# Performance work log

Measured on AMD Instinct MI355X. Metric: run time of the kernel, lower is better.

The kernel has to match this reference:

```python
import jax, jax.numpy as jnp
import numpy as np

N_NODES = 50000
N_EDGES = 800000
F_IN = 128
HIDDEN = 128
N_CLASSES = 10
N_GRAPHS = 256


def _glorot(key, shape):
    lim = float(np.sqrt(6.0 / (shape[0] + shape[1])))
    return jax.random.uniform(key, shape, jnp.float32, -lim, lim)


def setup_inputs() -> dict:
    key = jax.random.key(0)
    ks = jax.random.split(key, 12)
    x = jax.random.normal(ks[0], (N_NODES, F_IN), jnp.float32)
    edge_index = jax.random.randint(ks[1], (2, N_EDGES), 0, N_NODES, jnp.int64)
    batch = jnp.sort(jax.random.randint(ks[2], (N_NODES,), 0, N_GRAPHS, jnp.int64))
    dims = [(F_IN, HIDDEN), (HIDDEN, HIDDEN), (HIDDEN, N_CLASSES)]
    params = {}
    for i, (din, dout) in enumerate(dims, start=1):
        params[f"Wl{i}"] = _glorot(ks[2 + 2 * i], (din, dout))   # lin_l: applied to aggregated neighbors (has bias)
        params[f"bl{i}"] = jnp.zeros((dout,), jnp.float32)
        params[f"Wr{i}"] = _glorot(ks[3 + 2 * i], (din, dout))   # lin_r: applied to root/self features (no bias)
    return {"x": x, "edge_index": edge_index, "batch": batch, **params}


def _sage_conv(x, src, dst, Wl, bl, Wr):
    # mean aggregation of source features at destination nodes
    msg = x[src]                                                    # [E, D] gather
    ssum = jax.ops.segment_sum(msg, dst, num_segments=N_NODES)      # [N, D]
    cnt = jax.ops.segment_sum(jnp.ones((src.shape[0],), x.dtype), dst, num_segments=N_NODES)
    agg = ssum / jnp.maximum(cnt, 1.0)[:, None]
    return agg @ Wl + bl + x @ Wr


def reference(x, edge_index, batch, Wl1, bl1, Wr1, Wl2, bl2, Wr2, Wl3, bl3, Wr3):
    src, dst = edge_index[0], edge_index[1]
    h = _sage_conv(x, src, dst, Wl1, bl1, Wr1)
    h = _sage_conv(h, src, dst, Wl2, bl2, Wr2)
    h = _sage_conv(h, src, dst, Wl3, bl3, Wr3)                      # [N, C]
    # global mean pool over graphs
    gsum = jax.ops.segment_sum(h, batch, num_segments=N_GRAPHS)     # [G, C]
    gcnt = jax.ops.segment_sum(jnp.ones((h.shape[0],), h.dtype), batch, num_segments=N_GRAPHS)
    pooled = gsum / jnp.maximum(gcnt, 1.0)[:, None]
    return jax.nn.log_softmax(pooled, axis=-1)
```

## Files before the change

### kernel.cpp

```cpp
#include <hip/hip_runtime.h>


#define CAP 48
#define EB 4096

typedef __attribute__((ext_vector_type(8))) short short8;
typedef __attribute__((ext_vector_type(4))) float floatx4;

static __device__ __forceinline__ unsigned short f2bf(float f) {
    unsigned int u = __float_as_uint(f);
    u += 0x7FFFu + ((u >> 16) & 1u);
    return (unsigned short)(u >> 16);
}
static __device__ __forceinline__ float bf2f(unsigned short b) {
    return __uint_as_float(((unsigned int)b) << 16);
}

__global__ void prep_weights(const float* __restrict__ Wl2, const float* __restrict__ Wr2,
                             const float* __restrict__ Wl3, const float* __restrict__ Wr3,
                             float* __restrict__ m2Mg,
                             int* __restrict__ zero_base, int zero_words,
                             unsigned int* __restrict__ mmz, unsigned int* __restrict__ q2b32,
                             unsigned int* __restrict__ t3b32, int N,
                             const int* __restrict__ ei, int E, int ablk, int nbk,
                             unsigned int* __restrict__ bedges, int* __restrict__ runCnt) {
    __shared__ int hist[512];
    __shared__ float wtT_s[128 * 20];
    if (blockIdx.x < (unsigned)ablk) {
        for (int i = threadIdx.x; i < nbk; i += 256) hist[i] = 0;
        __syncthreads();
        int e0 = blockIdx.x * EB + threadIdx.x;
        unsigned int pk[16];
        int bk[16], loc[16];
#pragma unroll
        for (int k = 0; k < 16; ++k) {
            int e = e0 + k * 256;
            if (e < E) {
                int src = ei[e];
                int dst = ei[E + e];
                bk[k] = dst >> 7;
                pk[k] = ((unsigned int)(dst & 127) << 16) | (unsigned int)src;
                loc[k] = atomicAdd(&hist[bk[k]], 1);
            } else bk[k] = -1;
        }
        __syncthreads();
        for (int i = threadIdx.x; i < nbk; i += 256)
            runCnt[(size_t)blockIdx.x * nbk + i] = hist[i];
#pragma unroll
        for (int k = 0; k < 16; ++k)
            if (bk[k] >= 0 && loc[k] < CAP)
                bedges[((size_t)bk[k] * ablk + blockIdx.x) * CAP + loc[k]] = pk[k];
        return;
    }
    int rb = blockIdx.x - ablk;
    if (rb < 4) {
        const int tid = threadIdx.x;
        for (int i = tid; i < 2560; i += 256) {
            int f = i / 20, c = i - f * 20;
            wtT_s[i] = (c < 10) ? Wl3[f * 10 + c] : Wr3[f * 10 + (c - 10)];
        }
        __syncthreads();
        int jl = tid >> 3;
        int cg = tid & 7;
        int j = rb * 32 + jl;
        const float* w2row = ((cg < 4) ? Wl2 : Wr2) + (size_t)j * 128;
        int c20 = (cg & 3) * 5;
        float acc[5] = {0.f, 0.f, 0.f, 0.f, 0.f};
        for (int f4 = 0; f4 < 32; ++f4) {
            float4 wv = *(const float4*)&w2row[f4 * 4];
#pragma unroll
            for (int e = 0; e < 4; ++e) {
                float w = (e == 0) ? wv.x : (e == 1) ? wv.y : (e == 2) ? wv.z : wv.w;
                const float* wt = &wtT_s[(f4 * 4 + e) * 20 + c20];
#pragma unroll
                for (int i = 0; i < 5; ++i) acc[i] += w * wt[i];
            }
        }
        int cc = (cg >> 2) * 20 + c20;
#pragma unroll
        for (int i = 0; i < 5; ++i) m2Mg[j * 40 + cc + i] = acc[i];
        return;
    }
    if (rb == 4) {
        if (threadIdx.x < 20) mmz[(size_t)N * 20 + threadIdx.x] = 0;
        if (threadIdx.x >= 32 && threadIdx.x < 42)
            q2b32[(size_t)N * 10 + (threadIdx.x - 32)] = 0;
        if (threadIdx.x >= 64 && threadIdx.x < 74)
            t3b32[(size_t)N * 10 + (threadIdx.x - 64)] = 0;
        return;
    }
    int i = (rb - 5) * 256 + threadIdx.x;
    if (i < zero_words) zero_base[i] = 0;
}

__global__ __launch_bounds__(256) void prep2(
    const float* __restrict__ Wl1, const float* __restrict__ Wr1,
    const float* __restrict__ Wl3, const float* __restrict__ Wr3,
    const float* __restrict__ bl1, const float* __restrict__ bl2,
    const float* __restrict__ m2Mg, short* __restrict__ Wq,
    float* __restrict__ cbv) {
    __shared__ float m2s[128 * 40];
    const int tid = threadIdx.x;
    if (blockIdx.x == 8) {
        if (tid < 40) {
            float s = 0.f;
            if (tid < 20) {
                for (int k = 0; k < 128; ++k) s += bl1[k] * m2Mg[k * 40 + tid];
            } else {
                int c = tid - 20;
                for (int k = 0; k < 128; ++k) s += bl1[k] * m2Mg[k * 40 + 20 + c];
                for (int f = 0; f < 128; ++f) {
                    float wt = (c < 10) ? Wl3[f * 10 + c] : Wr3[f * 10 + (c - 10)];
                    s += bl2[f] * wt;
                }
            }
            cbv[tid] = s;
        }
        return;
    }
    for (int i = tid; i < 5120; i += 256) m2s[i] = m2Mg[i];
    __syncthreads();
    int rl = tid >> 3;
    int cg = tid & 7;
    int r = blockIdx.x * 32 + rl;
    int sh = r >> 7, k = r & 127;
    const float* wrow = (sh ? Wr1 : Wl1) + (size_t)k * 128;
    int c0 = cg * 5;
    float acc[5] = {0.f, 0.f, 0.f, 0.f, 0.f};
    for (int j4 = 0; j4 < 32; ++j4) {
        float4 wv = *(const float4*)&wrow[j4 * 4];
#pragma unroll
        for (int e = 0; e < 4; ++e) {
            float w = (e == 0) ? wv.x : (e == 1) ? wv.y : (e == 2) ? wv.z : wv.w;
            const float* mr = &m2s[(j4 * 4 + e) * 40 + c0];
#pragma unroll
            for (int i = 0; i < 5; ++i) acc[i] += w * mr[i];
        }
    }
    int ks = k >> 5, rem = k & 31, q = rem >> 3, jj = rem & 7;
#pragma unroll
    for (int i = 0; i < 5; ++i) {
        int f = sh * 40 + c0 + i;
        int mi = f >> 4, m = f & 15;
        int l = q * 16 + m;
        Wq[(((mi * 4 + ks) * 64) + l) * 8 + jj] = (short)f2bf(acc[i]);
    }
}

__global__ __launch_bounds__(256) void fillX(
    const float* __restrict__ x, const short* __restrict__ Wq,
    const float* __restrict__ cbv, unsigned short* __restrict__ mm,
    float* __restrict__ bmrow, int N, int nbk, int ablk,
    const unsigned int* __restrict__ bedges, const int* __restrict__ runCnt,
    int* __restrict__ cnt, unsigned short* __restrict__ colbuf) {
    __shared__ unsigned short As[64 * 136];
    __shared__ int lcnt[128];
    if (blockIdx.x >= (unsigned)nbk) {
        int blk = blockIdx.x - nbk;
        int node0 = blk * 64;
#pragma unroll
        for (int c = 0; c < 8; ++c) {
            int idx = c * 256 + threadIdx.x;
            int r = idx >> 5;
            int c4 = idx & 31;
            int row = node0 + r;
            float4 v = make_float4(0.f, 0.f, 0.f, 0.f);
            if (row < N) v = *(const float4*)&x[(size_t)row * 128 + c4 * 4];
            ushort4 p;
            p.x = f2bf(v.x); p.y = f2bf(v.y); p.z = f2bf(v.z); p.w = f2bf(v.w);
            *(ushort4*)&As[r * 136 + c4 * 4] = p;
        }
        __syncthreads();

        const int w = threadIdx.x >> 6;
        const int lane = threadIdx.x & 63;
        const int q = lane >> 4;
        const int m = lane & 15;

        floatx4 acc[5] = {};
#pragma unroll
        for (int s = 0; s < 4; ++s) {
            short8 bfrag = *(const short8*)&As[(w * 16 + m) * 136 + s * 32 + q * 8];
#pragma unroll
            for (int mi = 0; mi < 5; ++mi) {
                short8 wf = *(const short8*)&Wq[((mi * 4 + s) * 64 + lane) * 8];
                acc[mi] = __builtin_amdgcn_mfma_f32_16x16x32_bf16(
                    wf, bfrag, acc[mi], 0, 0, 0);
            }
        }
        int node = node0 + w * 16 + m;
        if (node < N) {
#pragma unroll
            for (int mi = 0; mi < 5; ++mi) {
                int f0 = mi * 16 + q * 4;
                floatx4 a = acc[mi];
                if (f0 < 40) {
                    ushort4 p;
                    p.x = f2bf(a[0]); p.y = f2bf(a[1]);
                    p.z = f2bf(a[2]); p.w = f2bf(a[3]);
                    *(ushort4*)&mm[(size_t)node * 40 + f0] = p;
                } else {
                    float4 cb = *(const float4*)&cbv[f0 - 40];
                    float4 o = make_float4(a[0] + cb.x, a[1] + cb.y,
                                           a[2] + cb.z, a[3] + cb.w);
                    *(float4*)&bmrow[(size_t)node * 40 + (f0 - 40)] = o;
                }
            }
        }
    } else {
        int b = blockIdx.x;
        if (threadIdx.x < 128) lcnt[threadIdx.x] = 0;
        __syncthreads();
        for (int blk = threadIdx.x; blk < ablk; blk += 256) {
            int c = runCnt[(size_t)blk * nbk + b];
            c = min(c, CAP);
            size_t ebase = ((size_t)b * ablk + blk) * CAP;
            for (int i = 0; i < c; ++i) {
                unsigned int pk = bedges[ebase + i];
                int dl = pk >> 16;
                int slot = atomicAdd(&lcnt[dl], 1);
                if (slot < CAP)
                    colbuf[(size_t)(b * 128 + dl) * CAP + slot] =
                        (unsigned short)(pk & 0xFFFFu);
            }
        }
        __syncthreads();
        int node = b * 128 + threadIdx.x;
        if (threadIdx.x < 128 && node < N) cnt[node] = lcnt[threadIdx.x];
    }
}

__global__ __launch_bounds__(256) void aggM(
    const uint2* __restrict__ mm2, const int* __restrict__ cnt,
    const unsigned short* __restrict__ colbuf, const float* __restrict__ bmrow,
    unsigned short* __restrict__ q2b, float* __restrict__ rbuf, int N) {
    const int lane = threadIdx.x & 63;
    const int wvi = threadIdx.x >> 6;
    const int la = lane & 15;
    const int qb = lane & 48;
    const int node = blockIdx.x * 16 + wvi * 4 + (lane >> 4);
    const bool valid = node < N;
    const int nodec = valid ? node : N - 1;
    const int deg = cnt[nodec];
    const int d = valid ? min(deg, CAP) : 0;
    const unsigned short* cb = colbuf + (size_t)nodec * CAP;

    float f0 = 0.f, f1 = 0.f, f2 = 0.f, f3 = 0.f;
    int nb = (d + 15) >> 4;
    for (int b = 0; b < nb; ++b) {
        int slot = b * 16 + la;
        int idx = (slot < d) ? (int)cb[slot] : N;
        uint2 vv[16];
#pragma unroll
        for (int j = 0; j < 16; ++j) {
            int s = __shfl(idx, qb + j, 64);
            uint2 z; z.x = 0u; z.y = 0u;
            vv[j] = (la < 10) ? mm2[(size_t)s * 10 + la] : z;
        }
#pragma unroll
        for (int j = 0; j < 16; ++j) {
            f0 += bf2f((unsigned short)(vv[j].x & 0xFFFF));
            f1 += bf2f((unsigned short)(vv[j].x >> 16));
            f2 += bf2f((unsigned short)(vv[j].y & 0xFFFF));
            f3 += bf2f((unsigned short)(vv[j].y >> 16));
        }
    }
    if (valid && la < 10) {
        float inv = 1.0f / (float)max(deg, 1);
        float4 bv = *(const float4*)&bmrow[(size_t)node * 40 + la * 4];
        float o0 = f0 * inv + bv.x, o1 = f1 * inv + bv.y;
        float o2 = f2 * inv + bv.z, o3 = f3 * inv + bv.w;
        if (la < 5) {
            ushort4 p;
            p.x = f2bf(o0); p.y = f2bf(o1); p.z = f2bf(o2); p.w = f2bf(o3);
            *(ushort4*)&q2b[(size_t)node * 20 + la * 4] = p;
        } else {
            *(float4*)&rbuf[(size_t)node * 20 + (la - 5) * 4] =
                make_float4(o0, o1, o2, o3);
        }
    }
}

__global__ __launch_bounds__(256) void agg20(
    const unsigned int* __restrict__ q2b32, const int* __restrict__ cnt,
    const unsigned short* __restrict__ colbuf, const float2* __restrict__ rbuf2,
    const float* __restrict__ bl3, unsigned int* __restrict__ t3b32, int N) {
    const int lane = threadIdx.x & 63;
    const int wvi = threadIdx.x >> 6;
    const int la = lane & 15;
    const int qb = lane & 48;
    const int node = blockIdx.x * 16 + wvi * 4 + (lane >> 4);
    const bool valid = node < N;
    const int nodec = valid ? node : N - 1;
    const int deg = cnt[nodec];
    const int d = valid ? min(deg, CAP) : 0;
    const unsigned short* cb = colbuf + (size_t)nodec * CAP;

    float f0 = 0.f, f1 = 0.f;
    int nb = (d + 15) >> 4;
    for (int b = 0; b < nb; ++b) {
        int slot = b * 16 + la;
        int idx = (slot < d) ? (int)cb[slot] : N;
        unsigned int vv[16];
#pragma unroll
        for (int j = 0; j < 16; ++j) {
            int s = __shfl(idx, qb + j, 64);
            vv[j] = (la < 10) ? q2b32[(size_t)s * 10 + la] : 0u;
        }
#pragma unroll
        for (int j = 0; j < 16; ++j) {
            f0 += bf2f((unsigned short)(vv[j] & 0xFFFF));
            f1 += bf2f((unsigned short)(vv[j] >> 16));
        }
    }
    if (valid && la < 10) {
        float inv = 1.0f / (float)max(deg, 1);
        float2 rv = rbuf2[(size_t)node * 10 + la];
        float v0 = f0 * inv + rv.x;
        float v1 = f1 * inv + rv.y;
        if (la < 5) { v0 += bl3[2 * la]; v1 += bl3[2 * la + 1]; }
        t3b32[(size_t)node * 10 + la] =
            (unsigned int)f2bf(v0) | ((unsigned int)f2bf(v1) << 16);
    }
}

__global__ __launch_bounds__(256) void agg10_pool(
    const unsigned short* __restrict__ t3b, const int* __restrict__ cnt,
    const unsigned short* __restrict__ colbuf, const float* __restrict__ bl3,
    const int* __restrict__ batch,
    float* __restrict__ gsum, float* __restrict__ gcnt, int N) {
    __shared__ float ls[2816];
    for (int i = threadIdx.x; i < 2816; i += 256) ls[i] = 0.f;
    __syncthreads();

    const int lane = threadIdx.x & 63;
    const int wvi = threadIdx.x >> 6;
    const int la = lane & 15;
    const int qb = lane & 48;
    const int node = blockIdx.x * 16 + wvi * 4 + (lane >> 4);
    const bool valid = node < N;
    const int nodec = valid ? node : N - 1;
    const int deg = cnt[nodec];
    const int d = valid ? min(deg, CAP) : 0;
    const unsigned short* cb = colbuf + (size_t)nodec * CAP;

    float acc = 0.f;
    int nb = (d + 15) >> 4;
    for (int b = 0; b < nb; ++b) {
        int slot = b * 16 + la;
        int idx = (slot < d) ? (int)cb[slot] : N;
        float vv[16];
#pragma unroll
        for (int j = 0; j < 16; ++j) {
            int s = __shfl(idx, qb + j, 64);
            vv[j] = (la < 10) ? bf2f(t3b[(size_t)s * 20 + la]) : 0.f;
        }
#pragma unroll
        for (int j = 0; j < 16; ++j) acc += vv[j];
    }
    if (valid && la < 10) {
        float self = bf2f(t3b[(size_t)node * 20 + 10 + la]);
        float h = (d > 0) ? (acc / (float)deg + self) : (bl3[la] + self);
        int g = batch[node];
        atomicAdd(&ls[g * 10 + la], h);
        if (la == 0) atomicAdd(&ls[2560 + g], 1.0f);
    }
    __syncthreads();
    for (int i = threadIdx.x; i < 2816; i += 256) {
        float v = ls[i];
        if (v != 0.f) {
            if (i < 2560) atomicAdd(&gsum[i], v);
            else          atomicAdd(&gcnt[i - 2560], v);
        }
    }
}

__global__ void finalize_pool(const float* __restrict__ gsum,
                              const float* __restrict__ gcnt,
                              float* __restrict__ out, int G) {
    int g = blockIdx.x * blockDim.x + threadIdx.x;
    if (g >= G) return;
    float inv = 1.0f / fmaxf(gcnt[g], 1.0f);
    float p[10];
    float m = -1e30f;
#pragma unroll
    for (int c = 0; c < 10; ++c) { p[c] = gsum[g * 10 + c] * inv; m = fmaxf(m, p[c]); }
    float s = 0.f;
#pragma unroll
    for (int c = 0; c < 10; ++c) s += expf(p[c] - m);
    float lse = logf(s);
#pragma unroll
    for (int c = 0; c < 10; ++c) out[g * 10 + c] = p[c] - m - lse;
}

extern "C" void kernel_launch(void* const* d_in, const int* in_sizes, int n_in,
                              void* d_out, int out_size, void* d_ws, size_t ws_size,
                              hipStream_t stream) {
    const float* x    = (const float*)d_in[0];
    const int*   ei   = (const int*)d_in[1];
    const int*   batch= (const int*)d_in[2];
    const float* Wl1  = (const float*)d_in[3];
    const float* bl1  = (const float*)d_in[4];
    const float* Wr1  = (const float*)d_in[5];
    const float* Wl2  = (const float*)d_in[6];
    const float* bl2  = (const float*)d_in[7];
    const float* Wr2  = (const float*)d_in[8];
    const float* Wl3  = (const float*)d_in[9];
    const float* bl3  = (const float*)d_in[10];
    const float* Wr3  = (const float*)d_in[11];
    float* out = (float*)d_out;

    const int N = in_sizes[2];
    const int E = in_sizes[1] / 2;
    const int G = out_size / 10;
    const int ablk = (E + EB - 1) / EB;
    const int nbk  = (N + 127) >> 7;

    char* ws = (char*)d_ws;
    size_t o = 0;
    float* gsum   = (float*)(ws + o); o += (size_t)G * 10 * 4;
    float* gcnt   = (float*)(ws + o); o += (size_t)G * 4;
    size_t zero_bytes = (o + 255) & ~(size_t)255;
    o = zero_bytes;
    int*            cnt    = (int*)(ws + o);            o += (size_t)N * 4;
    unsigned short* colbuf = (unsigned short*)(ws + o); o += ((size_t)N * CAP * 2 + 255) & ~(size_t)255;
    short*          Wq     = (short*)(ws + o);          o += (size_t)10240 * 2;
    float*          cbv    = (float*)(ws + o);          o += 40 * 4;
    o = (o + 255) & ~(size_t)255;
    float*          m2Mg   = (float*)(ws + o);          o += (size_t)128 * 40 * 4;
    unsigned short* mm     = (unsigned short*)(ws + o); o += (size_t)(N + 1) * 40 * 2;
    o = (o + 255) & ~(size_t)255;
    float*          bmrow  = (float*)(ws + o);          o += (size_t)N * 40 * 4;
    unsigned short* q2b    = (unsigned short*)(ws + o); o += (size_t)(N + 1) * 20 * 2;
    o = (o + 255) & ~(size_t)255;
    float*          rbuf   = (float*)(ws + o);          o += (size_t)N * 20 * 4;
    unsigned short* t3b    = (unsigned short*)(ws + o); o += (size_t)(N + 1) * 20 * 2;
    o = (o + 255) & ~(size_t)255;
    unsigned int*   bedges = (unsigned int*)(ws + o);   o += (size_t)nbk * ablk * CAP * 4;
    int*            runCnt = (int*)(ws + o);            o += (size_t)ablk * nbk * 4;

    int zero_words = (int)(zero_bytes / 4);
    int zblocks = (zero_words + 255) / 256;
    prep_weights<<<ablk + 5 + zblocks, 256, 0, stream>>>(
        Wl2, Wr2, Wl3, Wr3, m2Mg,
        (int*)ws, zero_words,
        (unsigned int*)mm, (unsigned int*)q2b, (unsigned int*)t3b, N,
        ei, E, ablk, nbk, bedges, runCnt);

    prep2<<<9, 256, 0, stream>>>(Wl1, Wr1, Wl3, Wr3, bl1, bl2, m2Mg, Wq, cbv);

    int gblocks = (N + 63) / 64;
    int ablocks = (N + 15) / 16;
    fillX<<<nbk + gblocks, 256, 0, stream>>>(x, Wq, cbv, mm, bmrow, N,
                                             nbk, ablk, bedges, runCnt,
                                             cnt, colbuf);
    aggM<<<ablocks, 256, 0, stream>>>((const uint2*)mm, cnt, colbuf,
                                      bmrow, q2b, rbuf, N);
    agg20<<<ablocks, 256, 0, stream>>>((const unsigned int*)q2b, cnt, colbuf,
                                       (const float2*)rbuf, bl3,
                                       (unsigned int*)t3b, N);
    agg10_pool<<<ablocks, 256, 0, stream>>>(t3b, cnt, colbuf, bl3, batch,
                                            gsum, gcnt, N);
    finalize_pool<<<1, 256, 0, stream>>>(gsum, gcnt, out, G);
}
```

Baseline: 190.8 us.

## Fold layer-2 linear maps to shrink gathered features from 40 to 20 columns

Re-associates the composed weight products so the first aggregation gathers a 20-wide bf16 projection per neighbor instead of 40 wide, and merges the combined left/right projection into the root-term columns of the packed MFMA weights. fillX now computes 4 MFMA tiles instead of 5, aggM writes a single 20-wide bf16 buffer, the separate float rbuf is dropped in favour of reading bmrow directly, and agg10_pool gathers packed bf16 pairs with 5 lanes instead of 10. The aim is to cut gather bandwidth and workspace traffic in the edge-aggregation kernels. The extra bf16 rounding on the folded products may shift numerics slightly.

```diff
diff --git a/kernel.cpp b/kernel.cpp
--- a/kernel.cpp
+++ b/kernel.cpp
@@ -20,7 +20,7 @@
                              const float* __restrict__ Wl3, const float* __restrict__ Wr3,
                              float* __restrict__ m2Mg,
                              int* __restrict__ zero_base, int zero_words,
-                             unsigned int* __restrict__ mmz, unsigned int* __restrict__ q2b32,
+                             unsigned int* __restrict__ mmz, unsigned int* __restrict__ zb32,
                              unsigned int* __restrict__ t3b32, int N,
                              const int* __restrict__ ei, int E, int ablk, int nbk,
                              unsigned int* __restrict__ bedges, int* __restrict__ runCnt) {
@@ -82,9 +82,9 @@
         return;
     }
     if (rb == 4) {
-        if (threadIdx.x < 20) mmz[(size_t)N * 20 + threadIdx.x] = 0;
+        if (threadIdx.x < 10) mmz[(size_t)N * 10 + threadIdx.x] = 0;
         if (threadIdx.x >= 32 && threadIdx.x < 42)
-            q2b32[(size_t)N * 10 + (threadIdx.x - 32)] = 0;
+            zb32[(size_t)N * 10 + (threadIdx.x - 32)] = 0;
         if (threadIdx.x >= 64 && threadIdx.x < 74)
             t3b32[(size_t)N * 10 + (threadIdx.x - 64)] = 0;
         return;
@@ -100,8 +100,15 @@
     const float* __restrict__ m2Mg, short* __restrict__ Wq,
     float* __restrict__ cbv) {
     __shared__ float m2s[128 * 40];
+    __shared__ float cL[32][20];
     const int tid = threadIdx.x;
-    if (blockIdx.x == 8) {
+    if (blockIdx.x == 4) {
+        for (int i = tid; i < 512; i += 256) {
+            int k = i >> 2, f = 60 + (i & 3);
+            int ks = k >> 5, rem = k & 31, qq = rem >> 3, jj = rem & 7;
+            int mi = f >> 4, m = f & 15, l = qq * 16 + m;
+            Wq[(((mi * 4 + ks) * 64) + l) * 8 + jj] = 0;
+        }
         if (tid < 40) {
             float s = 0.f;
             if (tid < 20) {
@@ -120,30 +127,48 @@
     }
     for (int i = tid; i < 5120; i += 256) m2s[i] = m2Mg[i];
     __syncthreads();
-    int rl = tid >> 3;
+    int kl = tid >> 3;
     int cg = tid & 7;
-    int r = blockIdx.x * 32 + rl;
-    int sh = r >> 7, k = r & 127;
-    const float* wrow = (sh ? Wr1 : Wl1) + (size_t)k * 128;
-    int c0 = cg * 5;
-    float acc[5] = {0.f, 0.f, 0.f, 0.f, 0.f};
+    int k = blockIdx.x * 32 + kl;
+    int c0 = (cg & 3) * 5;
+    bool left = (cg < 4);
+    const float* wrow = (left ? Wl1 : Wr1) + (size_t)k * 128;
+    float accM[5] = {0.f, 0.f, 0.f, 0.f, 0.f};
+    float accR[5] = {0.f, 0.f, 0.f, 0.f, 0.f};
     for (int j4 = 0; j4 < 32; ++j4) {
         float4 wv = *(const float4*)&wrow[j4 * 4];
 #pragma unroll
         for (int e = 0; e < 4; ++e) {
             float w = (e == 0) ? wv.x : (e == 1) ? wv.y : (e == 2) ? wv.z : wv.w;
-            const float* mr = &m2s[(j4 * 4 + e) * 40 + c0];
-#pragma unroll
-            for (int i = 0; i < 5; ++i) acc[i] += w * mr[i];
-        }
-    }
-    int ks = k >> 5, rem = k & 31, q = rem >> 3, jj = rem & 7;
+            const float* mr = &m2s[(j4 * 4 + e) * 40];
+#pragma unroll
+            for (int i = 0; i < 5; ++i) {
+                accM[i] += w * mr[c0 + i];
+                accR[i] += w * mr[20 + c0 + i];
+            }
+        }
+    }
+    if (left) {
+#pragma unroll
+        for (int i = 0; i < 5; ++i) cL[kl][c0 + i] = accR[i];
+    }
+    __syncthreads();
+    int ks = k >> 5, rem = k & 31, qq = rem >> 3, jj = rem & 7;
 #pragma unroll
     for (int i = 0; i < 5; ++i) {
-        int f = sh * 40 + c0 + i;
-        int mi = f >> 4, m = f & 15;
-        int l = q * 16 + m;
-        Wq[(((mi * 4 + ks) * 64) + l) * 8 + jj] = (short)f2bf(acc[i]);
+        if (left) {
+            int f = c0 + i;
+            int mi = f >> 4, m = f & 15, l = qq * 16 + m;
+            Wq[(((mi * 4 + ks) * 64) + l) * 8 + jj] = (short)f2bf(accM[i]);
+        } else {
+            int f = 20 + c0 + i;
+            int mi = f >> 4, m = f & 15, l = qq * 16 + m;
+            Wq[(((mi * 4 + ks) * 64) + l) * 8 + jj] =
+                (short)f2bf(accM[i] + cL[kl][c0 + i]);
+            int f2 = 40 + c0 + i;
+            int mi2 = f2 >> 4, m2 = f2 & 15, l2 = qq * 16 + m2;
+            Wq[(((mi2 * 4 + ks) * 64) + l2) * 8 + jj] = (short)f2bf(accR[i]);
+        }
     }
 }
 
@@ -177,12 +202,12 @@
         const int q = lane >> 4;
         const int m = lane & 15;
 
-        floatx4 acc[5] = {};
+        floatx4 acc[4] = {};
 #pragma unroll
         for (int s = 0; s < 4; ++s) {
             short8 bfrag = *(const short8*)&As[(w * 16 + m) * 136 + s * 32 + q * 8];
 #pragma unroll
-            for (int mi = 0; mi < 5; ++mi) {
+            for (int mi = 0; mi < 4; ++mi) {
                 short8 wf = *(const short8*)&Wq[((mi * 4 + s) * 64 + lane) * 8];
                 acc[mi] = __builtin_amdgcn_mfma_f32_16x16x32_bf16(
                     wf, bfrag, acc[mi], 0, 0, 0);
@@ -191,19 +216,19 @@
         int node = node0 + w * 16 + m;
         if (node < N) {
 #pragma unroll
-            for (int mi = 0; mi < 5; ++mi) {
+            for (int mi = 0; mi < 4; ++mi) {
                 int f0 = mi * 16 + q * 4;
                 floatx4 a = acc[mi];
-                if (f0 < 40) {
+                if (f0 < 20) {
                     ushort4 p;
                     p.x = f2bf(a[0]); p.y = f2bf(a[1]);
                     p.z = f2bf(a[2]); p.w = f2bf(a[3]);
-                    *(ushort4*)&mm[(size_t)node * 40 + f0] = p;
-                } else {
-                    float4 cb = *(const float4*)&cbv[f0 - 40];
+                    *(ushort4*)&mm[(size_t)node * 20 + f0] = p;
+                } else if (f0 < 60) {
+                    float4 cb = *(const float4*)&cbv[f0 - 20];
                     float4 o = make_float4(a[0] + cb.x, a[1] + cb.y,
                                            a[2] + cb.z, a[3] + cb.w);
-                    *(float4*)&bmrow[(size_t)node * 40 + (f0 - 40)] = o;
+                    *(float4*)&bmrow[(size_t)node * 40 + (f0 - 20)] = o;
                 }
             }
         }
@@ -231,9 +256,9 @@
 }
 
 __global__ __launch_bounds__(256) void aggM(
-    const uint2* __restrict__ mm2, const int* __restrict__ cnt,
-    const unsigned short* __restrict__ colbuf, const float* __restrict__ bmrow,
-    unsigned short* __restrict__ q2b, float* __restrict__ rbuf, int N) {
+    const unsigned int* __restrict__ mm32, const int* __restrict__ cnt,
+    const unsigned short* __restrict__ colbuf, const float2* __restrict__ bmrow2,
+    unsigned int* __restrict__ zb32, int N) {
     const int lane = threadIdx.x & 63;
     const int wvi = threadIdx.x >> 6;
     const int la = lane & 15;
@@ -245,45 +270,36 @@
     const int d = valid ? min(deg, CAP) : 0;
     const unsigned short* cb = colbuf + (size_t)nodec * CAP;
 
-    float f0 = 0.f, f1 = 0.f, f2 = 0.f, f3 = 0.f;
+    float f0 = 0.f, f1 = 0.f;
     int nb = (d + 15) >> 4;
     for (int b = 0; b < nb; ++b) {
         int slot = b * 16 + la;
         int idx = (slot < d) ? (int)cb[slot] : N;
-        uint2 vv[16];
+        unsigned int vv[16];
 #pragma unroll
         for (int j = 0; j < 16; ++j) {
             int s = __shfl(idx, qb + j, 64);
-            uint2 z; z.x = 0u; z.y = 0u;
-            vv[j] = (la < 10) ? mm2[(size_t)s * 10 + la] : z;
-        }
-#pragma unroll
-        for (int j = 0; j < 16; ++j) {
-            f0 += bf2f((unsigned short)(vv[j].x & 0xFFFF));
-            f1 += bf2f((unsigned short)(vv[j].x >> 16));
-            f2 += bf2f((unsigned short)(vv[j].y & 0xFFFF));
-            f3 += bf2f((unsigned short)(vv[j].y >> 16));
+            vv[j] = (la < 10) ? mm32[(size_t)s * 10 + la] : 0u;
+        }
+#pragma unroll
+        for (int j = 0; j < 16; ++j) {
+            f0 += bf2f((unsigned short)(vv[j] & 0xFFFF));
+            f1 += bf2f((unsigned short)(vv[j] >> 16));
         }
     }
     if (valid && la < 10) {
         float inv = 1.0f / (float)max(deg, 1);
-        float4 bv = *(const float4*)&bmrow[(size_t)node * 40 + la * 4];
-        float o0 = f0 * inv + bv.x, o1 = f1 * inv + bv.y;
-        float o2 = f2 * inv + bv.z, o3 = f3 * inv + bv.w;
-        if (la < 5) {
-            ushort4 p;
-            p.x = f2bf(o0); p.y = f2bf(o1); p.z = f2bf(o2); p.w = f2bf(o3);
-            *(ushort4*)&q2b[(size_t)node * 20 + la * 4] = p;
-        } else {
-            *(float4*)&rbuf[(size_t)node * 20 + (la - 5) * 4] =
-                make_float4(o0, o1, o2, o3);
-        }
+        float2 bp = bmrow2[(size_t)node * 20 + la];
+        float v0 = f0 * inv + bp.x;
+        float v1 = f1 * inv + bp.y;
+        zb32[(size_t)node * 10 + la] =
+            (unsigned int)f2bf(v0) | ((unsigned int)f2bf(v1) << 16);
     }
 }
 
 __global__ __launch_bounds__(256) void agg20(
-    const unsigned int* __restrict__ q2b32, const int* __restrict__ cnt,
-    const unsigned short* __restrict__ colbuf, const float2* __restrict__ rbuf2,
+    const unsigned int* __restrict__ zb32, const int* __restrict__ cnt,
+    const unsigned short* __restrict__ colbuf, const float2* __restrict__ bmrow2,
     const float* __restrict__ bl3, unsigned int* __restrict__ t3b32, int N) {
     const int lane = threadIdx.x & 63;
     const int wvi = threadIdx.x >> 6;
@@ -305,7 +321,7 @@
 #pragma unroll
         for (int j = 0; j < 16; ++j) {
             int s = __shfl(idx, qb + j, 64);
-            vv[j] = (la < 10) ? q2b32[(size_t)s * 10 + la] : 0u;
+            vv[j] = (la < 10) ? zb32[(size_t)s * 10 + la] : 0u;
         }
 #pragma unroll
         for (int j = 0; j < 16; ++j) {
@@ -315,7 +331,7 @@
     }
     if (valid && la < 10) {
         float inv = 1.0f / (float)max(deg, 1);
-        float2 rv = rbuf2[(size_t)node * 10 + la];
+        float2 rv = bmrow2[(size_t)node * 20 + 10 + la];
         float v0 = f0 * inv + rv.x;
         float v1 = f1 * inv + rv.y;
         if (la < 5) { v0 += bl3[2 * la]; v1 += bl3[2 * la + 1]; }
@@ -325,7 +341,7 @@
 }
 
 __global__ __launch_bounds__(256) void agg10_pool(
-    const unsigned short* __restrict__ t3b, const int* __restrict__ cnt,
+    const unsigned int* __restrict__ t3b32, const int* __restrict__ cnt,
     const unsigned short* __restrict__ colbuf, const float* __restrict__ bl3,
     const int* __restrict__ batch,
     float* __restrict__ gsum, float* __restrict__ gcnt, int N) {
@@ -344,25 +360,32 @@
     const int d = valid ? min(deg, CAP) : 0;
     const unsigned short* cb = colbuf + (size_t)nodec * CAP;
 
-    float acc = 0.f;
+    float acc0 = 0.f, acc1 = 0.f;
     int nb = (d + 15) >> 4;
     for (int b = 0; b < nb; ++b) {
         int slot = b * 16 + la;
         int idx = (slot < d) ? (int)cb[slot] : N;
-        float vv[16];
+        unsigned int vv[16];
 #pragma unroll
         for (int j = 0; j < 16; ++j) {
             int s = __shfl(idx, qb + j, 64);
-            vv[j] = (la < 10) ? bf2f(t3b[(size_t)s * 20 + la]) : 0.f;
-        }
-#pragma unroll
-        for (int j = 0; j < 16; ++j) acc += vv[j];
-    }
-    if (valid && la < 10) {
-        float self = bf2f(t3b[(size_t)node * 20 + 10 + la]);
-        float h = (d > 0) ? (acc / (float)deg + self) : (bl3[la] + self);
+            vv[j] = (la < 5) ? t3b32[(size_t)s * 10 + la] : 0u;
+        }
+#pragma unroll
+        for (int j = 0; j < 16; ++j) {
+            acc0 += bf2f((unsigned short)(vv[j] & 0xFFFF));
+            acc1 += bf2f((unsigned short)(vv[j] >> 16));
+        }
+    }
+    if (valid && la < 5) {
+        unsigned int sv = t3b32[(size_t)node * 10 + 5 + la];
+        float self0 = bf2f((unsigned short)(sv & 0xFFFF));
+        float self1 = bf2f((unsigned short)(sv >> 16));
+        float h0 = (d > 0) ? (acc0 / (float)deg + self0) : (bl3[2 * la] + self0);
+        float h1 = (d > 0) ? (acc1 / (float)deg + self1) : (bl3[2 * la + 1] + self1);
         int g = batch[node];
-        atomicAdd(&ls[g * 10 + la], h);
+        atomicAdd(&ls[g * 10 + 2 * la], h0);
+        atomicAdd(&ls[g * 10 + 2 * la + 1], h1);
         if (la == 0) atomicAdd(&ls[2560 + g], 1.0f);
     }
     __syncthreads();
@@ -424,16 +447,15 @@
     o = zero_bytes;
     int*            cnt    = (int*)(ws + o);            o += (size_t)N * 4;
     unsigned short* colbuf = (unsigned short*)(ws + o); o += ((size_t)N * CAP * 2 + 255) & ~(size_t)255;
-    short*          Wq     = (short*)(ws + o);          o += (size_t)10240 * 2;
+    short*          Wq     = (short*)(ws + o);          o += (size_t)8192 * 2;
     float*          cbv    = (float*)(ws + o);          o += 40 * 4;
     o = (o + 255) & ~(size_t)255;
     float*          m2Mg   = (float*)(ws + o);          o += (size_t)128 * 40 * 4;
-    unsigned short* mm     = (unsigned short*)(ws + o); o += (size_t)(N + 1) * 40 * 2;
+    unsigned short* mm     = (unsigned short*)(ws + o); o += (size_t)(N + 1) * 20 * 2;
     o = (o + 255) & ~(size_t)255;
     float*          bmrow  = (float*)(ws + o);          o += (size_t)N * 40 * 4;
-    unsigned short* q2b    = (unsigned short*)(ws + o); o += (size_t)(N + 1) * 20 * 2;
+    unsigned short* zb     = (unsigned short*)(ws + o); o += (size_t)(N + 1) * 20 * 2;
     o = (o + 255) & ~(size_t)255;
-    float*          rbuf   = (float*)(ws + o);          o += (size_t)N * 20 * 4;
     unsigned short* t3b    = (unsigned short*)(ws + o); o += (size_t)(N + 1) * 20 * 2;
     o = (o + 255) & ~(size_t)255;
     unsigned int*   bedges = (unsigned int*)(ws + o);   o += (size_t)nbk * ablk * CAP * 4;
@@ -444,22 +466,23 @@
     prep_weights<<<ablk + 5 + zblocks, 256, 0, stream>>>(
         Wl2, Wr2, Wl3, Wr3, m2Mg,
         (int*)ws, zero_words,
-        (unsigned int*)mm, (unsigned int*)q2b, (unsigned int*)t3b, N,
+        (unsigned int*)mm, (unsigned int*)zb, (unsigned int*)t3b, N,
         ei, E, ablk, nbk, bedges, runCnt);
 
-    prep2<<<9, 256, 0, stream>>>(Wl1, Wr1, Wl3, Wr3, bl1, bl2, m2Mg, Wq, cbv);
+    prep2<<<5, 256, 0, stream>>>(Wl1, Wr1, Wl3, Wr3, bl1, bl2, m2Mg, Wq, cbv);
 
     int gblocks = (N + 63) / 64;
     int ablocks = (N + 15) / 16;
     fillX<<<nbk + gblocks, 256, 0, stream>>>(x, Wq, cbv, mm, bmrow, N,
                                              nbk, ablk, bedges, runCnt,
                                              cnt, colbuf);
-    aggM<<<ablocks, 256, 0, stream>>>((const uint2*)mm, cnt, colbuf,
-                                      bmrow, q2b, rbuf, N);
-    agg20<<<ablocks, 256, 0, stream>>>((const unsigned int*)q2b, cnt, colbuf,
-                                       (const float2*)rbuf, bl3,
+    aggM<<<ablocks, 256, 0, stream>>>((const unsigned int*)mm, cnt, colbuf,
+                                      (const float2*)bmrow,
+                                      (unsigned int*)zb, N);
+    agg20<<<ablocks, 256, 0, stream>>>((const unsigned int*)zb, cnt, colbuf,
+                                       (const float2*)bmrow, bl3,
                                        (unsigned int*)t3b, N);
-    agg10_pool<<<ablocks, 256, 0, stream>>>(t3b, cnt, colbuf, bl3, batch,
-                                            gsum, gcnt, N);
+    agg10_pool<<<ablocks, 256, 0, stream>>>((const unsigned int*)t3b, cnt, colbuf,
+                                            bl3, batch, gsum, gcnt, N);
     finalize_pool<<<1, 256, 0, stream>>>(gsum, gcnt, out, G);
 }
```

Result: faster. 176.0 us (-7.7%).
